# Optimization experiments

Measured on AMD Instinct MI355X. Metric: run time of the kernel, lower is better.

The kernel has to match this reference:

```python
import jax, jax.numpy as jnp
import numpy as np

N, IN_DIM, OUT_DIM, H = 4096, 128, 128, 4
HEAD_DIM = OUT_DIM // H
NEG_SLOPE = 0.2


def setup_inputs() -> dict:
    key = jax.random.key(0)
    k1, k2, k3, k4, k5 = jax.random.split(key, 5)
    x = jax.random.normal(k1, (N, IN_DIM), dtype=jnp.float32)
    adj = jax.random.randint(k2, (N, N), 0, 2, dtype=jnp.int32)
    # nn.Linear(in_dim, out_dim, bias=False): weight is [out_dim, in_dim]
    W = jax.random.normal(k3, (OUT_DIM, IN_DIM), dtype=jnp.float32) * (1.0 / np.sqrt(IN_DIM))
    attn_src = jax.random.normal(k4, (1, H, HEAD_DIM), dtype=jnp.float32) * 0.1
    attn_dst = jax.random.normal(k5, (1, H, HEAD_DIM), dtype=jnp.float32) * 0.1
    return {"x": x, "adj": adj, "W": W, "attn_src": attn_src, "attn_dst": attn_dst}


def reference(x, adj, W, attn_src, attn_dst):
    n = x.shape[0]
    h = (x @ W.T).reshape(n, H, HEAD_DIM)            # [N, H, D]
    e_src = jnp.sum(h * attn_src, axis=-1)           # [N, H]
    e_dst = jnp.sum(h * attn_dst, axis=-1)           # [N, H]
    e = e_src[:, None, :] + e_dst[None, :, :]        # [N, N, H]
    e = jax.nn.leaky_relu(e, negative_slope=NEG_SLOPE)
    e = jnp.where((adj == 0)[:, :, None], -jnp.inf, e)
    alpha = jax.nn.softmax(e, axis=1)                # softmax over neighbors j
    # dropout omitted (eval mode)
    out = jnp.einsum('ijh,jhd->ihd', alpha, h)       # [N, H, D]
    return out.reshape(n, -1)
```

## Files before the change

kernel.cpp:

```cpp
#include <hip/hip_runtime.h>
#include <hip/hip_bf16.h>

#define NN 4096
#define SJ 8
#define JCH (NN / SJ)
#define JSTEP 128
#define NSTEPS (JCH / JSTEP)
#define LOG2E 1.44269504f

typedef __attribute__((ext_vector_type(4))) float f32x4;
typedef __attribute__((ext_vector_type(4))) int i32x4;
typedef __attribute__((ext_vector_type(4))) unsigned int u32x4;
typedef __attribute__((ext_vector_type(8))) short short8;

__device__ __forceinline__ unsigned pk2(float a, float b) {
    float2 t; t.x = a; t.y = b;
    __hip_bfloat162 h = __float22bfloat162_rn(t);
    unsigned r;
    __builtin_memcpy(&r, &h, 4);
    return r;
}

__device__ __forceinline__ short8 load8_bf(const float* __restrict__ p) {
    f32x4 a = *(const f32x4*)p;
    f32x4 b = *(const f32x4*)(p + 4);
    u32x4 v = {pk2(a[0], a[1]), pk2(a[2], a[3]), pk2(b[0], b[1]), pk2(b[2], b[3])};
    return __builtin_bit_cast(short8, v);
}

__global__ __launch_bounds__(256) void k1_proj(
        const float* __restrict__ x, const float* __restrict__ W,
        const float* __restrict__ asrc, const float* __restrict__ adst,
        unsigned short* __restrict__ hT, float* __restrict__ Rt,
        float* __restrict__ Bt, float* __restrict__ Dt) {
    const int ibase = blockIdx.x * 16;
    const int w = threadIdx.x >> 6;
    const int lane = threadIdx.x & 63;
    const int grp = lane >> 4, li = lane & 15;

    const float* xrow = x + (ibase + li) * 128;
    const float* w0 = W + (w * 32 + li) * 128;
    const float* w1 = W + (w * 32 + 16 + li) * 128;

    f32x4 c0 = {0.f, 0.f, 0.f, 0.f}, c1 = {0.f, 0.f, 0.f, 0.f};
#pragma unroll
    for (int ko = 0; ko < 128; ko += 32) {
        const int kk = ko + grp * 8;
        short8 a = load8_bf(xrow + kk);
        short8 b0 = load8_bf(w0 + kk);
        short8 b1 = load8_bf(w1 + kk);
        c0 = __builtin_amdgcn_mfma_f32_16x16x32_bf16(a, b0, c0, 0, 0, 0);
        c1 = __builtin_amdgcn_mfma_f32_16x16x32_bf16(a, b1, c1, 0, 0, 0);
    }
    const float as0 = asrc[w * 32 + li], as1 = asrc[w * 32 + 16 + li];
    const float ad0 = adst[w * 32 + li], ad1 = adst[w * 32 + 16 + li];
    float pes[4], ped[4];
#pragma unroll
    for (int r = 0; r < 4; ++r) {
        pes[r] = c0[r] * as0 + c1[r] * as1;
        ped[r] = c0[r] * ad0 + c1[r] * ad1;
    }
#pragma unroll
    for (int m = 1; m < 16; m <<= 1) {
#pragma unroll
        for (int r = 0; r < 4; ++r) {
            pes[r] += __shfl_xor(pes[r], m);
            ped[r] += __shfl_xor(ped[r], m);
        }
    }
    if (li == 0) {
#pragma unroll
        for (int r = 0; r < 4; ++r) {
            const int row = ibase + grp * 4 + r;
            Rt[w * NN + row] = __builtin_amdgcn_exp2f(-0.8f * LOG2E * pes[r]);
            Bt[w * NN + row] = __builtin_amdgcn_exp2f(LOG2E * ped[r]);
            Dt[w * NN + row] = __builtin_amdgcn_exp2f(0.2f * LOG2E * ped[r]);
        }
    }
#pragma unroll
    for (int r = 0; r < 4; ++r) {
        const int row = ibase + grp * 4 + r;
        hT[(w * 32 + li) * NN + row] = (unsigned short)__builtin_bit_cast(unsigned short, __float2bfloat16(c0[r]));
        hT[(w * 32 + 16 + li) * NN + row] = (unsigned short)__builtin_bit_cast(unsigned short, __float2bfloat16(c1[r]));
    }
}

__device__ __forceinline__ short8 buildQ(float R,
                                         const f32x4 B0, const f32x4 B1,
                                         const f32x4 D0, const f32x4 D1,
                                         const i32x4 alo, const i32x4 ahi) {
    float p[8];
#pragma unroll
    for (int e = 0; e < 4; ++e) {
        float m = fmaxf(B0[e], R * D0[e]);
        unsigned bits = __builtin_bit_cast(unsigned, m) & (0u - (unsigned)alo[e]);
        p[e] = __builtin_bit_cast(float, bits);
    }
#pragma unroll
    for (int e = 0; e < 4; ++e) {
        float m = fmaxf(B1[e], R * D1[e]);
        unsigned bits = __builtin_bit_cast(unsigned, m) & (0u - (unsigned)ahi[e]);
        p[4 + e] = __builtin_bit_cast(float, bits);
    }
    u32x4 u = {pk2(p[0], p[1]), pk2(p[2], p[3]), pk2(p[4], p[5]), pk2(p[6], p[7])};
    return __builtin_bit_cast(short8, u);
}

__global__ __launch_bounds__(256) void k3_main(
        const int* __restrict__ adj, const unsigned short* __restrict__ hT,
        const float* __restrict__ Rt, const float* __restrict__ Bt,
        const float* __restrict__ Dt,
        float* __restrict__ numer, float* __restrict__ denom) {
    __shared__ unsigned int adjbuf[2][32 * 128];

    const int ibase = blockIdx.x * 32;
    const int jstart = blockIdx.y * JCH;
    const int head = threadIdx.x >> 6;
    const int lane = threadIdx.x & 63;
    const int grp = lane >> 4, li = lane & 15;
    const int sub = lane >> 5, p = lane & 31;

    const float R0 = Rt[head * NN + ibase + li];
    const float R1 = Rt[head * NN + ibase + 16 + li];
    const float* Bp = Bt + head * NN;
    const float* Dp = Dt + head * NN;
    const unsigned short* h0 = hT + (head * 32 + li) * NN;
    const unsigned short* h1 = hT + (head * 32 + 16 + li) * NN;
    const unsigned int* adju = (const unsigned int*)adj;

    f32x4 c00 = {0.f,0.f,0.f,0.f}, c01 = {0.f,0.f,0.f,0.f};
    f32x4 c10 = {0.f,0.f,0.f,0.f}, c11 = {0.f,0.f,0.f,0.f};
    f32x4 dn0 = {0.f,0.f,0.f,0.f}, dn1 = {0.f,0.f,0.f,0.f};
    short8 bones;
#pragma unroll
    for (int e = 0; e < 8; ++e) bones[e] = (short)0x3F80;

    auto stage = [&](unsigned int* dst, int jb) {
#pragma unroll
        for (int k = 0; k < 4; ++k) {
            const int R = head * 8 + k * 2 + sub;
            const int c = p ^ (R & 31);
            const unsigned int* g = adju + (size_t)(ibase + R) * NN + jb + c * 4;
            __builtin_amdgcn_global_load_lds(g, dst + (head * 8 + k * 2) * 128, 16, 0, 0);
        }
    };

    unsigned int* cur = &adjbuf[0][0];
    unsigned int* nxt = &adjbuf[1][0];

    stage(cur, jstart);
    __syncthreads();

    for (int t = 0; t < NSTEPS; ++t) {
        const int jb = jstart + t * JSTEP;
        if (t + 1 < NSTEPS) stage(nxt, jb + JSTEP);

#pragma unroll
        for (int ks = 0; ks < 4; ++ks) {
            const int j0 = jb + ks * 32 + grp * 8;
            const f32x4 Bv0 = *(const f32x4*)(Bp + j0);
            const f32x4 Bv1 = *(const f32x4*)(Bp + j0 + 4);
            const f32x4 Dv0 = *(const f32x4*)(Dp + j0);
            const f32x4 Dv1 = *(const f32x4*)(Dp + j0 + 4);
            const short8 b0 = *(const short8*)(h0 + j0);
            const short8 b1 = *(const short8*)(h1 + j0);

            const int cb = ks * 8 + grp * 2;
            const i32x4 q00 = *(const i32x4*)&cur[li * 128 + (cb ^ li) * 4];
            const i32x4 q01 = *(const i32x4*)&cur[li * 128 + ((cb + 1) ^ li) * 4];
            const i32x4 q10 = *(const i32x4*)&cur[(li + 16) * 128 + (cb ^ (li + 16)) * 4];
            const i32x4 q11 = *(const i32x4*)&cur[(li + 16) * 128 + ((cb + 1) ^ (li + 16)) * 4];

            const short8 A0 = buildQ(R0, Bv0, Bv1, Dv0, Dv1, q00, q01);
            const short8 A1 = buildQ(R1, Bv0, Bv1, Dv0, Dv1, q10, q11);

            c00 = __builtin_amdgcn_mfma_f32_16x16x32_bf16(A0, b0, c00, 0, 0, 0);
            c01 = __builtin_amdgcn_mfma_f32_16x16x32_bf16(A0, b1, c01, 0, 0, 0);
            c10 = __builtin_amdgcn_mfma_f32_16x16x32_bf16(A1, b0, c10, 0, 0, 0);
            c11 = __builtin_amdgcn_mfma_f32_16x16x32_bf16(A1, b1, c11, 0, 0, 0);
            dn0 = __builtin_amdgcn_mfma_f32_16x16x32_bf16(A0, bones, dn0, 0, 0, 0);
            dn1 = __builtin_amdgcn_mfma_f32_16x16x32_bf16(A1, bones, dn1, 0, 0, 0);
        }

        __syncthreads();
        unsigned int* tmp = cur; cur = nxt; nxt = tmp;
    }

    const int r0 = ibase + grp * 4;
    float* nb = numer + head * 32 + li;
#pragma unroll
    for (int r = 0; r < 4; ++r) {
        atomicAdd(nb + (size_t)(r0 + r) * 128, c00[r]);
        atomicAdd(nb + (size_t)(r0 + r) * 128 + 16, c01[r]);
        atomicAdd(nb + (size_t)(r0 + 16 + r) * 128, c10[r]);
        atomicAdd(nb + (size_t)(r0 + 16 + r) * 128 + 16, c11[r]);
    }
    if (li == 0) {
#pragma unroll
        for (int r = 0; r < 4; ++r) {
            atomicAdd(denom + (r0 + r) * 4 + head, dn0[r]);
            atomicAdd(denom + (r0 + 16 + r) * 4 + head, dn1[r]);
        }
    }
}

__global__ __launch_bounds__(256) void k4_fin(const float* __restrict__ numer,
                                              const float* __restrict__ denom,
                                              float* __restrict__ out) {
    const int idx = blockIdx.x * 256 + threadIdx.x;
    const int node = idx >> 7;
    const int headc = (idx & 127) >> 5;
    out[idx] = numer[idx] / denom[node * 4 + headc];
}

extern "C" void kernel_launch(void* const* d_in, const int* in_sizes, int n_in,
                              void* d_out, int out_size, void* d_ws, size_t ws_size,
                              hipStream_t stream) {
    const float* x = (const float*)d_in[0];
    const int* adj = (const int*)d_in[1];
    const float* W = (const float*)d_in[2];
    const float* asrc = (const float*)d_in[3];
    const float* adst = (const float*)d_in[4];
    float* out = (float*)d_out;

    char* ws = (char*)d_ws;
    float* numer = (float*)ws;
    float* denom = (float*)(ws + (size_t)2097152);
    float* Rt = (float*)(ws + (size_t)2097152 + 65536);
    float* Bt = (float*)(ws + (size_t)2097152 + 131072);
    float* Dt = (float*)(ws + (size_t)2097152 + 196608);
    unsigned short* hT = (unsigned short*)(ws + (size_t)2097152 + 262144);

    (void)hipMemsetAsync(numer, 0, 2097152 + 65536, stream);
    k1_proj<<<256, 256, 0, stream>>>(x, W, asrc, adst, hT, Rt, Bt, Dt);
    k3_main<<<dim3(128, SJ), 256, 0, stream>>>(adj, hT, Rt, Bt, Dt, numer, denom);
    k4_fin<<<2048, 256, 0, stream>>>(numer, denom, out);
}
```

Measured before the change: 68.54 us.

## Triple-buffer adjacency tiles, widen row tile to 64, prefetch operands in registers

The main attention kernel now handles 64 query rows per block instead of 32, which halves the grid and reuses each loaded h/B/D operand across four row groups. Adjacency staging moves from a double buffer to a triple-buffered LDS ring of 64-column steps, using explicit vmcnt waits and raw barriers. The next step's h, B and D register operands are prefetched one iteration ahead. The projection kernel transposes its h output through shared memory so global stores are vectorised rather than scattered 2-byte writes. In exchange, register pressure rises (launch bounds request 2 blocks per SM), there are fewer blocks, and the hand-counted vmcnt waits are fragile.

```diff
diff --git a/kernel.cpp b/kernel.cpp
--- a/kernel.cpp
+++ b/kernel.cpp
@@ -4,8 +4,9 @@
 #define NN 4096
 #define SJ 8
 #define JCH (NN / SJ)
-#define JSTEP 128
+#define JSTEP 64
 #define NSTEPS (JCH / JSTEP)
+#define ROWS 64
 #define LOG2E 1.44269504f
 
 typedef __attribute__((ext_vector_type(4))) float f32x4;
@@ -33,6 +34,7 @@
         const float* __restrict__ asrc, const float* __restrict__ adst,
         unsigned short* __restrict__ hT, float* __restrict__ Rt,
         float* __restrict__ Bt, float* __restrict__ Dt) {
+    __shared__ unsigned short ttile[4][32][16];
     const int ibase = blockIdx.x * 16;
     const int w = threadIdx.x >> 6;
     const int lane = threadIdx.x & 63;
@@ -77,129 +79,168 @@
             Dt[w * NN + row] = __builtin_amdgcn_exp2f(0.2f * LOG2E * ped[r]);
         }
     }
-#pragma unroll
-    for (int r = 0; r < 4; ++r) {
-        const int row = ibase + grp * 4 + r;
-        hT[(w * 32 + li) * NN + row] = (unsigned short)__builtin_bit_cast(unsigned short, __float2bfloat16(c0[r]));
-        hT[(w * 32 + 16 + li) * NN + row] = (unsigned short)__builtin_bit_cast(unsigned short, __float2bfloat16(c1[r]));
-    }
-}
+    unsigned short* tw = &ttile[w][0][0];
+    {
+        uint2 v0; v0.x = pk2(c0[0], c0[1]); v0.y = pk2(c0[2], c0[3]);
+        uint2 v1; v1.x = pk2(c1[0], c1[1]); v1.y = pk2(c1[2], c1[3]);
+        *(uint2*)&tw[li * 16 + grp * 4] = v0;
+        *(uint2*)&tw[(li + 16) * 16 + grp * 4] = v1;
+    }
+    __syncthreads();
+    const int d = lane >> 1, half = lane & 1;
+    u32x4 v = *(const u32x4*)&ttile[w][d][half * 8];
+    *(u32x4*)(hT + (size_t)(w * 32 + d) * NN + ibase + half * 8) = v;
+}
+
+struct SR {
+    short8 t00, t01, t10, t11;
+    f32x4 B0a, B0b, B1a, B1b;
+    f32x4 D0a, D0b, D1a, D1b;
+};
 
 __device__ __forceinline__ short8 buildQ(float R,
-                                         const f32x4 B0, const f32x4 B1,
-                                         const f32x4 D0, const f32x4 D1,
-                                         const i32x4 alo, const i32x4 ahi) {
+                                         const f32x4 Ba, const f32x4 Bb,
+                                         const f32x4 Da, const f32x4 Db,
+                                         const i32x4 q0, const i32x4 q1) {
     float p[8];
 #pragma unroll
     for (int e = 0; e < 4; ++e) {
-        float m = fmaxf(B0[e], R * D0[e]);
-        unsigned bits = __builtin_bit_cast(unsigned, m) & (0u - (unsigned)alo[e]);
-        p[e] = __builtin_bit_cast(float, bits);
+        const float m = fmaxf(Ba[e], R * Da[e]);
+        p[e] = __builtin_bit_cast(float, __builtin_bit_cast(unsigned, m) & (0u - (unsigned)q0[e]));
     }
 #pragma unroll
     for (int e = 0; e < 4; ++e) {
-        float m = fmaxf(B1[e], R * D1[e]);
-        unsigned bits = __builtin_bit_cast(unsigned, m) & (0u - (unsigned)ahi[e]);
-        p[4 + e] = __builtin_bit_cast(float, bits);
+        const float m = fmaxf(Bb[e], R * Db[e]);
+        p[4 + e] = __builtin_bit_cast(float, __builtin_bit_cast(unsigned, m) & (0u - (unsigned)q1[e]));
     }
     u32x4 u = {pk2(p[0], p[1]), pk2(p[2], p[3]), pk2(p[4], p[5]), pk2(p[6], p[7])};
     return __builtin_bit_cast(short8, u);
 }
 
-__global__ __launch_bounds__(256) void k3_main(
+__global__ __launch_bounds__(256, 2) void k3_main(
         const int* __restrict__ adj, const unsigned short* __restrict__ hT,
         const float* __restrict__ Rt, const float* __restrict__ Bt,
         const float* __restrict__ Dt,
         float* __restrict__ numer, float* __restrict__ denom) {
-    __shared__ unsigned int adjbuf[2][32 * 128];
-
-    const int ibase = blockIdx.x * 32;
+    __shared__ unsigned int adjbuf[3][ROWS * 64];
+
+    const int ibase = blockIdx.x * ROWS;
     const int jstart = blockIdx.y * JCH;
     const int head = threadIdx.x >> 6;
     const int lane = threadIdx.x & 63;
     const int grp = lane >> 4, li = lane & 15;
-    const int sub = lane >> 5, p = lane & 31;
-
-    const float R0 = Rt[head * NN + ibase + li];
-    const float R1 = Rt[head * NN + ibase + 16 + li];
+
+    float Rv[4];
+#pragma unroll
+    for (int g = 0; g < 4; ++g) Rv[g] = Rt[head * NN + ibase + g * 16 + li];
+    const unsigned short* h0 = hT + (size_t)(head * 32 + li) * NN;
+    const unsigned short* h1 = hT + (size_t)(head * 32 + 16 + li) * NN;
     const float* Bp = Bt + head * NN;
     const float* Dp = Dt + head * NN;
-    const unsigned short* h0 = hT + (head * 32 + li) * NN;
-    const unsigned short* h1 = hT + (head * 32 + 16 + li) * NN;
     const unsigned int* adju = (const unsigned int*)adj;
 
-    f32x4 c00 = {0.f,0.f,0.f,0.f}, c01 = {0.f,0.f,0.f,0.f};
-    f32x4 c10 = {0.f,0.f,0.f,0.f}, c11 = {0.f,0.f,0.f,0.f};
-    f32x4 dn0 = {0.f,0.f,0.f,0.f}, dn1 = {0.f,0.f,0.f,0.f};
+    f32x4 c[4][2], dn[4];
+#pragma unroll
+    for (int g = 0; g < 4; ++g) {
+        c[g][0] = f32x4{0.f,0.f,0.f,0.f};
+        c[g][1] = f32x4{0.f,0.f,0.f,0.f};
+        dn[g] = f32x4{0.f,0.f,0.f,0.f};
+    }
     short8 bones;
 #pragma unroll
     for (int e = 0; e < 8; ++e) bones[e] = (short)0x3F80;
 
-    auto stage = [&](unsigned int* dst, int jb) {
+    auto stage = [&](int slot, int jb) {
 #pragma unroll
         for (int k = 0; k < 4; ++k) {
-            const int R = head * 8 + k * 2 + sub;
-            const int c = p ^ (R & 31);
-            const unsigned int* g = adju + (size_t)(ibase + R) * NN + jb + c * 4;
-            __builtin_amdgcn_global_load_lds(g, dst + (head * 8 + k * 2) * 128, 16, 0, 0);
+            const int Rw = head * 16 + k * 4 + grp;
+            const int cc = li ^ (Rw & 15);
+            const unsigned int* g = adju + (size_t)(ibase + Rw) * NN + jb + cc * 4;
+            __builtin_amdgcn_global_load_lds(g, &adjbuf[slot][(head * 16 + k * 4) * 64], 16, 0, 0);
         }
     };
-
-    unsigned int* cur = &adjbuf[0][0];
-    unsigned int* nxt = &adjbuf[1][0];
-
-    stage(cur, jstart);
-    __syncthreads();
-
+    auto loadR = [&](int jb) {
+        SR r;
+        r.t00 = *(const short8*)(h0 + jb + grp * 8);
+        r.t01 = *(const short8*)(h0 + jb + 32 + grp * 8);
+        r.t10 = *(const short8*)(h1 + jb + grp * 8);
+        r.t11 = *(const short8*)(h1 + jb + 32 + grp * 8);
+        r.B0a = *(const f32x4*)(Bp + jb + grp * 8);
+        r.B0b = *(const f32x4*)(Bp + jb + grp * 8 + 4);
+        r.B1a = *(const f32x4*)(Bp + jb + 32 + grp * 8);
+        r.B1b = *(const f32x4*)(Bp + jb + 32 + grp * 8 + 4);
+        r.D0a = *(const f32x4*)(Dp + jb + grp * 8);
+        r.D0b = *(const f32x4*)(Dp + jb + grp * 8 + 4);
+        r.D1a = *(const f32x4*)(Dp + jb + 32 + grp * 8);
+        r.D1b = *(const f32x4*)(Dp + jb + 32 + grp * 8 + 4);
+        return r;
+    };
+    auto compute = [&](const unsigned int* buf, const SR& S) {
+#pragma unroll
+        for (int ks = 0; ks < 2; ++ks) {
+            const short8 tA = ks ? S.t01 : S.t00;
+            const short8 tB = ks ? S.t11 : S.t10;
+            const f32x4 Ba = ks ? S.B1a : S.B0a;
+            const f32x4 Bb = ks ? S.B1b : S.B0b;
+            const f32x4 Da = ks ? S.D1a : S.D0a;
+            const f32x4 Db = ks ? S.D1b : S.D0b;
+            const int cb = ks * 8 + grp * 2;
+#pragma unroll
+            for (int g = 0; g < 4; ++g) {
+                const int row = li + g * 16;
+                const i32x4 q0 = *(const i32x4*)&buf[row * 64 + (cb ^ li) * 4];
+                const i32x4 q1 = *(const i32x4*)&buf[row * 64 + ((cb + 1) ^ li) * 4];
+                const short8 A = buildQ(Rv[g], Ba, Bb, Da, Db, q0, q1);
+                c[g][0] = __builtin_amdgcn_mfma_f32_16x16x32_bf16(A, tA, c[g][0], 0, 0, 0);
+                c[g][1] = __builtin_amdgcn_mfma_f32_16x16x32_bf16(A, tB, c[g][1], 0, 0, 0);
+                dn[g] = __builtin_amdgcn_mfma_f32_16x16x32_bf16(A, bones, dn[g], 0, 0, 0);
+            }
+        }
+    };
+
+    SR S[2];
+    stage(0, jstart);
+    S[0] = loadR(jstart);
+    stage(1, jstart + JSTEP);
+    asm volatile("s_waitcnt vmcnt(4)" ::: "memory");
+    __builtin_amdgcn_s_barrier();
+    __builtin_amdgcn_sched_barrier(0);
+
+#pragma unroll
     for (int t = 0; t < NSTEPS; ++t) {
-        const int jb = jstart + t * JSTEP;
-        if (t + 1 < NSTEPS) stage(nxt, jb + JSTEP);
-
-#pragma unroll
-        for (int ks = 0; ks < 4; ++ks) {
-            const int j0 = jb + ks * 32 + grp * 8;
-            const f32x4 Bv0 = *(const f32x4*)(Bp + j0);
-            const f32x4 Bv1 = *(const f32x4*)(Bp + j0 + 4);
-            const f32x4 Dv0 = *(const f32x4*)(Dp + j0);
-            const f32x4 Dv1 = *(const f32x4*)(Dp + j0 + 4);
-            const short8 b0 = *(const short8*)(h0 + j0);
-            const short8 b1 = *(const short8*)(h1 + j0);
-
-            const int cb = ks * 8 + grp * 2;
-            const i32x4 q00 = *(const i32x4*)&cur[li * 128 + (cb ^ li) * 4];
-            const i32x4 q01 = *(const i32x4*)&cur[li * 128 + ((cb + 1) ^ li) * 4];
-            const i32x4 q10 = *(const i32x4*)&cur[(li + 16) * 128 + (cb ^ (li + 16)) * 4];
-            const i32x4 q11 = *(const i32x4*)&cur[(li + 16) * 128 + ((cb + 1) ^ (li + 16)) * 4];
-
-            const short8 A0 = buildQ(R0, Bv0, Bv1, Dv0, Dv1, q00, q01);
-            const short8 A1 = buildQ(R1, Bv0, Bv1, Dv0, Dv1, q10, q11);
-
-            c00 = __builtin_amdgcn_mfma_f32_16x16x32_bf16(A0, b0, c00, 0, 0, 0);
-            c01 = __builtin_amdgcn_mfma_f32_16x16x32_bf16(A0, b1, c01, 0, 0, 0);
-            c10 = __builtin_amdgcn_mfma_f32_16x16x32_bf16(A1, b0, c10, 0, 0, 0);
-            c11 = __builtin_amdgcn_mfma_f32_16x16x32_bf16(A1, b1, c11, 0, 0, 0);
-            dn0 = __builtin_amdgcn_mfma_f32_16x16x32_bf16(A0, bones, dn0, 0, 0, 0);
-            dn1 = __builtin_amdgcn_mfma_f32_16x16x32_bf16(A1, bones, dn1, 0, 0, 0);
-        }
-
-        __syncthreads();
-        unsigned int* tmp = cur; cur = nxt; nxt = tmp;
-    }
-
-    const int r0 = ibase + grp * 4;
+        if (t + 1 < NSTEPS) S[(t + 1) & 1] = loadR(jstart + (t + 1) * JSTEP);
+        if (t + 2 < NSTEPS) stage((t + 2) % 3, jstart + (t + 2) * JSTEP);
+
+        compute(&adjbuf[t % 3][0], S[t & 1]);
+
+        if (t + 2 < NSTEPS) {
+            asm volatile("s_waitcnt vmcnt(4)" ::: "memory");
+        } else if (t + 1 < NSTEPS) {
+            asm volatile("s_waitcnt vmcnt(0)" ::: "memory");
+        }
+        if (t + 1 < NSTEPS) {
+            __builtin_amdgcn_s_barrier();
+            __builtin_amdgcn_sched_barrier(0);
+        }
+    }
+
     float* nb = numer + head * 32 + li;
 #pragma unroll
-    for (int r = 0; r < 4; ++r) {
-        atomicAdd(nb + (size_t)(r0 + r) * 128, c00[r]);
-        atomicAdd(nb + (size_t)(r0 + r) * 128 + 16, c01[r]);
-        atomicAdd(nb + (size_t)(r0 + 16 + r) * 128, c10[r]);
-        atomicAdd(nb + (size_t)(r0 + 16 + r) * 128 + 16, c11[r]);
+    for (int g = 0; g < 4; ++g) {
+        const int r0 = ibase + g * 16 + grp * 4;
+#pragma unroll
+        for (int r = 0; r < 4; ++r) {
+            atomicAdd(nb + (size_t)(r0 + r) * 128, c[g][0][r]);
+            atomicAdd(nb + (size_t)(r0 + r) * 128 + 16, c[g][1][r]);
+        }
     }
     if (li == 0) {
 #pragma unroll
-        for (int r = 0; r < 4; ++r) {
-            atomicAdd(denom + (r0 + r) * 4 + head, dn0[r]);
-            atomicAdd(denom + (r0 + 16 + r) * 4 + head, dn1[r]);
+        for (int g = 0; g < 4; ++g) {
+            const int r0 = ibase + g * 16 + grp * 4;
+#pragma unroll
+            for (int r = 0; r < 4; ++r)
+                atomicAdd(denom + (r0 + r) * 4 + head, dn[g][r]);
         }
     }
 }
@@ -233,6 +274,6 @@
 
     (void)hipMemsetAsync(numer, 0, 2097152 + 65536, stream);
     k1_proj<<<256, 256, 0, stream>>>(x, W, asrc, adst, hT, Rt, Bt, Dt);
-    k3_main<<<dim3(128, SJ), 256, 0, stream>>>(adj, hT, Rt, Bt, Dt, numer, denom);
+    k3_main<<<dim3(NN / ROWS, SJ), 256, 0, stream>>>(adj, hT, Rt, Bt, Dt, numer, denom);
     k4_fin<<<2048, 256, 0, stream>>>(numer, denom, out);
 }
```

Measured after the change: 61.58 us. -10.2%, faster.
